# Performance work log

Hardware: AMD Instinct MI355X
Metric: run time of the kernel (lower is better)

The kernel has to match this reference:

```python
import jax, jax.numpy as jnp
import numpy as np

B, S, D_IN, D_OUT, H = 4, 2048, 1024, 1024, 16
HD = D_OUT // H


def setup_inputs() -> dict:
    key = jax.random.key(0)
    ks = jax.random.split(key, 6)
    s_in = 1.0 / np.sqrt(D_IN)
    s_out = 1.0 / np.sqrt(D_OUT)
    return {
        "x": jax.random.normal(ks[0], (B, S, D_IN), dtype=jnp.float32),
        "Wq": jax.random.uniform(ks[1], (D_IN, D_OUT), jnp.float32, -s_in, s_in),
        "Wk": jax.random.uniform(ks[2], (D_IN, D_OUT), jnp.float32, -s_in, s_in),
        "Wv": jax.random.uniform(ks[3], (D_IN, D_OUT), jnp.float32, -s_in, s_in),
        "Wo": jax.random.uniform(ks[4], (D_OUT, D_OUT), jnp.float32, -s_out, s_out),
        "bo": jax.random.uniform(ks[5], (D_OUT,), jnp.float32, -s_out, s_out),
    }


def reference(x, Wq, Wk, Wv, Wo, bo):
    b, s, _ = x.shape
    # project and split heads: (b, h, s, hd)
    def heads(w):
        return (x @ w).reshape(b, s, H, HD).transpose(0, 2, 1, 3)
    q, k, v = heads(Wq), heads(Wk), heads(Wv)
    scores = jnp.einsum("bhqd,bhkd->bhqk", q, k) / np.sqrt(HD).astype(np.float32)
    causal = jnp.tril(jnp.ones((s, s), dtype=bool))  # True = keep
    scores = jnp.where(causal, scores, -jnp.inf)
    attn = jax.nn.softmax(scores, axis=-1)
    ctx = jnp.einsum("bhqk,bhkd->bhqd", attn, v)
    ctx = ctx.transpose(0, 2, 1, 3).reshape(b, s, D_OUT)
    return ctx @ Wo.T + bo
```

## Files before the change

### kernel.cpp

```cpp
#include <hip/hip_runtime.h>
#include <hip/hip_bf16.h>

#define BB   4
#define SS   2048
#define DIN  1024
#define DOUT 1024
#define NH   16
#define HDIM 64

typedef __hip_bfloat16 bf16;
typedef __attribute__((ext_vector_type(8))) short short8;
typedef __attribute__((ext_vector_type(4))) float floatx4;

#define AS1(p) ((const __attribute__((address_space(1))) void*)(p))
#define AS3(p) ((__attribute__((address_space(3))) void*)(p))

__global__ void prep_all_kernel(const float* __restrict__ x,
                                const float* __restrict__ Wq, const float* __restrict__ Wk,
                                const float* __restrict__ Wv, const float* __restrict__ Wo,
                                bf16* __restrict__ xb, bf16* __restrict__ wt,
                                bf16* __restrict__ wob) {
    __shared__ float tile[64][65];
    const int bid = blockIdx.x;
    const int tid = threadIdx.x;
    if (bid < 4096 || bid >= 4864) {
        const float* src = (bid < 4096) ? x : Wo;
        bf16* dst        = (bid < 4096) ? xb : wob;
        const int  rb    = (bid < 4096) ? bid : (bid - 4864);
        size_t i = ((size_t)rb * 256 + tid) * 8;
        float4 a = *(const float4*)(src + i);
        float4 b = *(const float4*)(src + i + 4);
        bf16 o[8] __attribute__((aligned(16)));
        o[0] = __float2bfloat16(a.x); o[1] = __float2bfloat16(a.y);
        o[2] = __float2bfloat16(a.z); o[3] = __float2bfloat16(a.w);
        o[4] = __float2bfloat16(b.x); o[5] = __float2bfloat16(b.y);
        o[6] = __float2bfloat16(b.z); o[7] = __float2bfloat16(b.w);
        *(short8*)(dst + i) = *(short8*)o;
        return;
    }
    const int pb = bid - 4096;
    const int kt = pb & 15;
    const int nt = pb >> 4;
    const int k0 = kt * 64, n0 = nt * 64;
    const float* W = (n0 < 1024) ? Wq : (n0 < 2048 ? Wk : Wv);
    const int col0 = n0 & 1023;
    {
        const int kl = tid >> 2, nc = (tid & 3) * 16;
        const float* src = W + (size_t)(k0 + kl) * 1024 + col0 + nc;
        #pragma unroll
        for (int i = 0; i < 16; i += 4) {
            float4 v = *(const float4*)(src + i);
            tile[kl][nc + i + 0] = v.x; tile[kl][nc + i + 1] = v.y;
            tile[kl][nc + i + 2] = v.z; tile[kl][nc + i + 3] = v.w;
        }
    }
    __syncthreads();
    {
        const int nl = tid >> 2, kc = (tid & 3) * 16;
        bf16 o[16] __attribute__((aligned(16)));
        #pragma unroll
        for (int i = 0; i < 16; ++i) o[i] = __float2bfloat16(tile[kc + i][nl]);
        bf16* dst = wt + (size_t)(n0 + nl) * 1024 + k0 + kc;
        *(short8*)dst       = *(short8*)&o[0];
        *(short8*)(dst + 8) = *(short8*)&o[8];
    }
}

template<int EPI>
__global__ __launch_bounds__(256) void gemm_bt_kernel(
    const bf16* __restrict__ A, const bf16* __restrict__ Bt,
    void* __restrict__ C, const float* __restrict__ bias, int K, int ldc,
    bf16* __restrict__ vt) {
    __shared__ __align__(16) bf16 As[2][128][64];
    __shared__ __align__(16) bf16 Bs[2][128][64];
    const int tid  = threadIdx.x;
    const int wave = tid >> 6, lane = tid & 63;
    const int lm   = lane & 15, quad = lane >> 4;
    const int wm   = (wave >> 1) * 64, wn = (wave & 1) * 64;
    const size_t rowA0 = (size_t)blockIdx.x * 128;
    const size_t rowB0 = (size_t)blockIdx.y * 128;

    const int srow8  = lane >> 3;
    const int schunk = (lane & 7) ^ srow8;
    const int sw     = lm & 7;

    floatx4 acc[4][4] = {};

    #pragma unroll
    for (int j = 0; j < 4; ++j) {
        const int rbase = (wave * 4 + j) * 8;
        const bf16* gA = A  + (rowA0 + rbase + srow8) * (size_t)K + schunk * 8;
        __builtin_amdgcn_global_load_lds(AS1(gA), AS3(&As[0][rbase][0]), 16, 0, 0);
        const bf16* gB = Bt + (rowB0 + rbase + srow8) * (size_t)K + schunk * 8;
        __builtin_amdgcn_global_load_lds(AS1(gB), AS3(&Bs[0][rbase][0]), 16, 0, 0);
    }

    const int nk = K >> 6;
    #pragma unroll 1
    for (int t = 0; t < nk; ++t) {
        const int cur = t & 1;
        __syncthreads();
        if (t + 1 < nk) {
            #pragma unroll
            for (int j = 0; j < 4; ++j) {
                const int rbase = (wave * 4 + j) * 8;
                const bf16* gA = A  + (rowA0 + rbase + srow8) * (size_t)K + (t + 1) * 64 + schunk * 8;
                __builtin_amdgcn_global_load_lds(AS1(gA), AS3(&As[cur ^ 1][rbase][0]), 16, 0, 0);
                const bf16* gB = Bt + (rowB0 + rbase + srow8) * (size_t)K + (t + 1) * 64 + schunk * 8;
                __builtin_amdgcn_global_load_lds(AS1(gB), AS3(&Bs[cur ^ 1][rbase][0]), 16, 0, 0);
            }
        }
        short8 a[4][2], b[4][2];
        #pragma unroll
        for (int i = 0; i < 4; ++i) {
            const int r = wm + i * 16 + lm;
            a[i][0] = *(const short8*)&As[cur][r][((quad    ) ^ sw) * 8];
            a[i][1] = *(const short8*)&As[cur][r][((quad + 4) ^ sw) * 8];
        }
        #pragma unroll
        for (int j = 0; j < 4; ++j) {
            const int r = wn + j * 16 + lm;
            b[j][0] = *(const short8*)&Bs[cur][r][((quad    ) ^ sw) * 8];
            b[j][1] = *(const short8*)&Bs[cur][r][((quad + 4) ^ sw) * 8];
        }
        __builtin_amdgcn_s_setprio(1);
        #pragma unroll
        for (int i = 0; i < 4; ++i)
            #pragma unroll
            for (int j = 0; j < 4; ++j) {
                acc[i][j] = __builtin_amdgcn_mfma_f32_16x16x32_bf16(a[i][0], b[j][0], acc[i][j], 0, 0, 0);
                acc[i][j] = __builtin_amdgcn_mfma_f32_16x16x32_bf16(a[i][1], b[j][1], acc[i][j], 0, 0, 0);
            }
        __builtin_amdgcn_s_setprio(0);
    }

    if (EPI == 0 && rowB0 >= 2048) {
        #pragma unroll
        for (int i = 0; i < 4; ++i) {
            size_t row = rowA0 + wm + i * 16 + quad * 4;
            const size_t b = row >> 11;
            const int    s = (int)(row & 2047);
            #pragma unroll
            for (int j = 0; j < 4; ++j) {
                const int col = (int)(rowB0 - 2048) + wn + j * 16 + lm;
                bf16 o[4] __attribute__((aligned(8)));
                #pragma unroll
                for (int r = 0; r < 4; ++r) o[r] = __float2bfloat16(acc[i][j][r]);
                *(uint64_t*)(vt + ((b * 16 + (col >> 6)) * 64 + (col & 63)) * (size_t)SS + s)
                    = *(uint64_t*)o;
            }
        }
        return;
    }

    #pragma unroll
    for (int i = 0; i < 4; ++i) {
        size_t row = rowA0 + wm + i * 16 + quad * 4;
        #pragma unroll
        for (int j = 0; j < 4; ++j) {
            size_t col = rowB0 + wn + j * 16 + lm;
            float bv = (EPI == 1) ? bias[col] : 0.0f;
            #pragma unroll
            for (int r = 0; r < 4; ++r) {
                if (EPI == 0)
                    ((bf16*)C)[(row + r) * ldc + col] = __float2bfloat16(acc[i][j][r]);
                else
                    ((float*)C)[(row + r) * ldc + col] = acc[i][j][r] + bv;
            }
        }
    }
}

#define PSTR 68
__global__ __launch_bounds__(256, 3) void flash_attn_kernel(
    const bf16* __restrict__ qkv, const bf16* __restrict__ vt, bf16* __restrict__ ctx) {
    __shared__ __align__(16) bf16 Ks[2][64 * 64];
    __shared__ __align__(16) bf16 Vs[2][64 * 64];
    __shared__ __align__(16) bf16 Pl[4][32 * PSTR + 8];
    const int tid  = threadIdx.x;
    const int wave = tid >> 6, lane = tid & 63;
    const int lm   = lane & 15, quad = lane >> 4;

    const int id  = blockIdx.x;
    const int jl  = (id >> 3) & 7;
    const int bh  = (id & 7) * 8 + jl;
    const int p   = 15 - (id >> 6);
    const int b = bh >> 4, h = bh & 15;

    const int lane8r = lane >> 3;
    const int schunk = (lane & 7) ^ lane8r;

    const bf16* kg = qkv + (size_t)b * SS * 3072 + 1024 + h * 64 + schunk * 8;
    const bf16* vg = vt + (size_t)(b * NH + h) * 64 * SS + schunk * 8;

    bf16* Pw = &Pl[wave][0];

    const int qb = p * 128 + wave * 32;
    const int nkt = 2 * p + 2;

    short8 bq[2][2];
    #pragma unroll
    for (int g = 0; g < 2; ++g) {
        const bf16* qp = qkv + ((size_t)(b * SS + qb + g * 16 + lm)) * 3072 + h * 64 + quad * 8;
        bq[g][0] = *(const short8*)qp;
        bq[g][1] = *(const short8*)(qp + 32);
    }

    floatx4 o[2][4] = {};
    float lsum[2] = {0.f, 0.f};

    #pragma unroll
    for (int c = 0; c < 2; ++c) {
        const int row = c * 32 + wave * 8 + lane8r;
        __builtin_amdgcn_global_load_lds(AS1(kg + (size_t)row * 3072), AS3(&Ks[0][(c * 256 + wave * 64) * 8]), 16, 0, 0);
        __builtin_amdgcn_global_load_lds(AS1(vg + (size_t)row * SS), AS3(&Vs[0][(c * 256 + wave * 64) * 8]), 16, 0, 0);
    }

    #pragma unroll 1
    for (int kt = 0; kt < nkt; ++kt) {
        const int cur = kt & 1;
        __syncthreads();
        if (kt + 1 < nkt) {
            #pragma unroll
            for (int c = 0; c < 2; ++c) {
                const int row = c * 32 + wave * 8 + lane8r;
                __builtin_amdgcn_global_load_lds(AS1(kg + (size_t)((kt + 1) * 64 + row) * 3072),
                                                 AS3(&Ks[cur ^ 1][(c * 256 + wave * 64) * 8]), 16, 0, 0);
                __builtin_amdgcn_global_load_lds(AS1(vg + (size_t)row * SS + (kt + 1) * 64),
                                                 AS3(&Vs[cur ^ 1][(c * 256 + wave * 64) * 8]), 16, 0, 0);
            }
        }

        if (kt * 64 > qb + 31) continue;

        const int sw = lm & 7;
        const bf16* Ksb = &Ks[cur][0];
        const bf16* Vsb = &Vs[cur][0];
        short8 ka[4][2], va[4][2];
        #pragma unroll
        for (int nt = 0; nt < 4; ++nt) {
            const int r0 = (nt * 16 + lm) * 64;
            ka[nt][0] = *(const short8*)(Ksb + r0 + ((quad ^ sw) * 8));
            ka[nt][1] = *(const short8*)(Ksb + r0 + (((4 + quad) ^ sw) * 8));
            va[nt][0] = *(const short8*)(Vsb + r0 + ((quad ^ sw) * 8));
            va[nt][1] = *(const short8*)(Vsb + r0 + (((4 + quad) ^ sw) * 8));
        }

        #pragma unroll
        for (int g = 0; g < 2; ++g) {
            floatx4 sc[4];
            __builtin_amdgcn_s_setprio(1);
            #pragma unroll
            for (int nt = 0; nt < 4; ++nt) {
                floatx4 z = {};
                z = __builtin_amdgcn_mfma_f32_16x16x32_bf16(ka[nt][0], bq[g][0], z, 0, 0, 0);
                z = __builtin_amdgcn_mfma_f32_16x16x32_bf16(ka[nt][1], bq[g][1], z, 0, 0, 0);
                sc[nt] = z;
            }
            __builtin_amdgcn_s_setprio(0);
            if (kt * 64 + 63 > qb + g * 16) {
                const int qrow = qb + g * 16 + lm;
                #pragma unroll
                for (int nt = 0; nt < 4; ++nt)
                    #pragma unroll
                    for (int r = 0; r < 4; ++r)
                        if (kt * 64 + nt * 16 + quad * 4 + r > qrow) sc[nt][r] = -1e30f;
            }
            #pragma unroll
            for (int nt = 0; nt < 4; ++nt) {
                bf16 pk[4] __attribute__((aligned(8)));
                #pragma unroll
                for (int r = 0; r < 4; ++r) {
                    float pv = __builtin_amdgcn_exp2f(sc[nt][r] * 0.18033688f);
                    lsum[g] += pv;
                    pk[r] = __float2bfloat16(pv);
                }
                *(uint64_t*)&Pw[(g * 16 + lm) * PSTR + nt * 16 + quad * 4] = *(uint64_t*)pk;
            }
        }
        #pragma unroll
        for (int g = 0; g < 2; ++g) {
            const short8 ap0 = *(const short8*)&Pw[(g * 16 + lm) * PSTR + quad * 8];
            const short8 ap1 = *(const short8*)&Pw[(g * 16 + lm) * PSTR + 32 + quad * 8];
            __builtin_amdgcn_s_setprio(1);
            #pragma unroll
            for (int t = 0; t < 4; ++t) {
                o[g][t] = __builtin_amdgcn_mfma_f32_16x16x32_bf16(ap0, va[t][0], o[g][t], 0, 0, 0);
                o[g][t] = __builtin_amdgcn_mfma_f32_16x16x32_bf16(ap1, va[t][1], o[g][t], 0, 0, 0);
            }
            __builtin_amdgcn_s_setprio(0);
        }
    }

    #pragma unroll
    for (int g = 0; g < 2; ++g) {
        float rsum = lsum[g];
        rsum += __shfl_xor(rsum, 16);
        rsum += __shfl_xor(rsum, 32);
        float rl[4];
        #pragma unroll
        for (int r = 0; r < 4; ++r) rl[r] = 1.0f / __shfl(rsum, quad * 4 + r);
        #pragma unroll
        for (int t = 0; t < 4; ++t)
            #pragma unroll
            for (int r = 0; r < 4; ++r) {
                size_t row = (size_t)b * SS + qb + g * 16 + quad * 4 + r;
                ctx[row * 1024 + h * 64 + t * 16 + lm] = __float2bfloat16(o[g][t][r] * rl[r]);
            }
    }
}

extern "C" void kernel_launch(void* const* d_in, const int* in_sizes, int n_in,
                              void* d_out, int out_size, void* d_ws, size_t ws_size,
                              hipStream_t stream) {
    const float* x  = (const float*)d_in[0];
    const float* Wq = (const float*)d_in[1];
    const float* Wk = (const float*)d_in[2];
    const float* Wv = (const float*)d_in[3];
    const float* Wo = (const float*)d_in[4];
    const float* bo = (const float*)d_in[5];

    char* ws = (char*)d_ws;
    bf16* xb  = (bf16*)ws;  ws += (size_t)8192 * 1024 * 2;
    bf16* wt  = (bf16*)ws;  ws += (size_t)3072 * 1024 * 2;
    bf16* wob = (bf16*)ws;  ws += (size_t)1024 * 1024 * 2;
    bf16* qkv = (bf16*)ws;  ws += (size_t)8192 * 3072 * 2;
    bf16* vtb = (bf16*)ws;  ws += (size_t)BB * NH * HDIM * SS * 2;
    bf16* ctx = xb;

    prep_all_kernel<<<5376, 256, 0, stream>>>(x, Wq, Wk, Wv, Wo, xb, wt, wob);
    gemm_bt_kernel<0><<<dim3(64, 24), 256, 0, stream>>>(xb, wt, (void*)qkv, nullptr, 1024, 3072, vtb);
    flash_attn_kernel<<<1024, 256, 0, stream>>>(qkv, vtb, ctx);
    gemm_bt_kernel<1><<<dim3(64, 8), 256, 0, stream>>>(ctx, wob, d_out, bo, 1024, 1024, nullptr);
}
```

Before: 249.8 us.

## Load K/V tiles directly from global memory per wave, dropping LDS staging

Each wave now loads its K and V fragments straight from global memory into registers instead of staging them cooperatively in double-buffered LDS with global_load_lds and block-wide barriers. Without the shared staging, the per-iteration __syncthreads is gone, and each wave runs its own causal trip count instead of skipping tiles. A dummy shared pad array keeps the LDS footprint and occupancy about the same. The cost is redundant global/L2 traffic: the four waves each fetch the same K/V tiles, and access is strided per lane rather than coalesced.

```diff
diff --git a/kernel.cpp b/kernel.cpp
--- a/kernel.cpp
+++ b/kernel.cpp
@@ -174,12 +174,13 @@
 #define PSTR 68
 __global__ __launch_bounds__(256, 3) void flash_attn_kernel(
     const bf16* __restrict__ qkv, const bf16* __restrict__ vt, bf16* __restrict__ ctx) {
-    __shared__ __align__(16) bf16 Ks[2][64 * 64];
-    __shared__ __align__(16) bf16 Vs[2][64 * 64];
     __shared__ __align__(16) bf16 Pl[4][32 * PSTR + 8];
+    __shared__ char pad_[30720];
     const int tid  = threadIdx.x;
     const int wave = tid >> 6, lane = tid & 63;
     const int lm   = lane & 15, quad = lane >> 4;
+
+    if (__builtin_expect(((size_t)ctx & 1) != 0, 0)) pad_[tid] = (char)lane;
 
     const int id  = blockIdx.x;
     const int jl  = (id >> 3) & 7;
@@ -187,16 +188,13 @@
     const int p   = 15 - (id >> 6);
     const int b = bh >> 4, h = bh & 15;
 
-    const int lane8r = lane >> 3;
-    const int schunk = (lane & 7) ^ lane8r;
-
-    const bf16* kg = qkv + (size_t)b * SS * 3072 + 1024 + h * 64 + schunk * 8;
-    const bf16* vg = vt + (size_t)(b * NH + h) * 64 * SS + schunk * 8;
+    const bf16* kg = qkv + (size_t)b * SS * 3072 + 1024 + h * 64;
+    const bf16* vg = vt + (size_t)(b * NH + h) * 64 * SS;
 
     bf16* Pw = &Pl[wave][0];
 
-    const int qb = p * 128 + wave * 32;
-    const int nkt = 2 * p + 2;
+    const int qb  = p * 128 + wave * 32;
+    const int nkt = 2 * p + 1 + (wave >> 1);
 
     short8 bq[2][2];
     #pragma unroll
@@ -209,41 +207,17 @@
     floatx4 o[2][4] = {};
     float lsum[2] = {0.f, 0.f};
 
-    #pragma unroll
-    for (int c = 0; c < 2; ++c) {
-        const int row = c * 32 + wave * 8 + lane8r;
-        __builtin_amdgcn_global_load_lds(AS1(kg + (size_t)row * 3072), AS3(&Ks[0][(c * 256 + wave * 64) * 8]), 16, 0, 0);
-        __builtin_amdgcn_global_load_lds(AS1(vg + (size_t)row * SS), AS3(&Vs[0][(c * 256 + wave * 64) * 8]), 16, 0, 0);
-    }
-
     #pragma unroll 1
     for (int kt = 0; kt < nkt; ++kt) {
-        const int cur = kt & 1;
-        __syncthreads();
-        if (kt + 1 < nkt) {
-            #pragma unroll
-            for (int c = 0; c < 2; ++c) {
-                const int row = c * 32 + wave * 8 + lane8r;
-                __builtin_amdgcn_global_load_lds(AS1(kg + (size_t)((kt + 1) * 64 + row) * 3072),
-                                                 AS3(&Ks[cur ^ 1][(c * 256 + wave * 64) * 8]), 16, 0, 0);
-                __builtin_amdgcn_global_load_lds(AS1(vg + (size_t)row * SS + (kt + 1) * 64),
-                                                 AS3(&Vs[cur ^ 1][(c * 256 + wave * 64) * 8]), 16, 0, 0);
-            }
-        }
-
-        if (kt * 64 > qb + 31) continue;
-
-        const int sw = lm & 7;
-        const bf16* Ksb = &Ks[cur][0];
-        const bf16* Vsb = &Vs[cur][0];
         short8 ka[4][2], va[4][2];
         #pragma unroll
         for (int nt = 0; nt < 4; ++nt) {
-            const int r0 = (nt * 16 + lm) * 64;
-            ka[nt][0] = *(const short8*)(Ksb + r0 + ((quad ^ sw) * 8));
-            ka[nt][1] = *(const short8*)(Ksb + r0 + (((4 + quad) ^ sw) * 8));
-            va[nt][0] = *(const short8*)(Vsb + r0 + ((quad ^ sw) * 8));
-            va[nt][1] = *(const short8*)(Vsb + r0 + (((4 + quad) ^ sw) * 8));
+            const bf16* kr = kg + (size_t)(kt * 64 + nt * 16 + lm) * 3072 + quad * 8;
+            ka[nt][0] = *(const short8*)kr;
+            ka[nt][1] = *(const short8*)(kr + 32);
+            const bf16* vr = vg + (size_t)(nt * 16 + lm) * SS + kt * 64 + quad * 8;
+            va[nt][0] = *(const short8*)vr;
+            va[nt][1] = *(const short8*)(vr + 32);
         }
 
         #pragma unroll
```

New measurement: 310.4 us. 1.24x slower.
